# Kernel tuning notes

Hardware: AMD Instinct MI355X
Metric: run time of the kernel (lower is better)

Reference implementation:

```python
import jax, jax.numpy as jnp
import numpy as np

B, S, H, D = 2, 2048, 16, 128  # batch, seq, n_head, head_dim; n_embd = H*D
N_EMBD = H * D

def setup_inputs() -> dict:
    key = jax.random.key(0)
    kq, kk, kv = jax.random.split(key, 3)
    q = jax.random.normal(kq, (B, S, H, D), dtype=jnp.float32)
    k = jax.random.normal(kk, (B, S, H, D), dtype=jnp.float32)
    v = jax.random.normal(kv, (B, S, H, D), dtype=jnp.float32)
    return {"q": q, "k": k, "v": v}

def reference(q, k, v):
    # [B,S,H,D] -> [B,H,S,D]
    qh = jnp.transpose(q, (0, 2, 1, 3))
    kh = jnp.transpose(k, (0, 2, 1, 3))
    vh = jnp.transpose(v, (0, 2, 1, 3))
    # scores scaled by head_dim (NOT sqrt), matching the original module
    att = jnp.einsum('bhqd,bhkd->bhqk', qh, kh) / D
    att = jax.nn.softmax(att, axis=-1)
    y = jnp.einsum('bhqk,bhkd->bhqd', att, vh)
    # [B,H,S,D] -> [B,S,H,D] -> [B*S, n_embd]
    y = jnp.transpose(y, (0, 2, 1, 3)).reshape(B * S, N_EMBD)
    return y
```

## Files before the change

kernel.cpp:

```cpp
#include <hip/hip_runtime.h>


#define SEQ   2048
#define NHEAD 16
#define DH    128
#define NB    2
#define BQ    64
#define BK    64
#define NWAVE 4
#define NTHR  256
#define VSTR  72
#define PSTR  40
#define NKV   (SEQ / BK)
#define NELEM (NB * SEQ * NHEAD * DH)

typedef __attribute__((ext_vector_type(8))) short bf16x8;
typedef __attribute__((ext_vector_type(4))) float f32x4;

__device__ __forceinline__ unsigned short f2bf(float x) {
    unsigned int u = __builtin_bit_cast(unsigned int, x);
    u += 0x7fffu + ((u >> 16) & 1u);
    return (unsigned short)(u >> 16);
}

__global__ __launch_bounds__(256) void cvt_bf16(
    const float* __restrict__ q, const float* __restrict__ k,
    const float* __restrict__ v, unsigned short* __restrict__ dst)
{
    const int y = blockIdx.y;
    const float* s = (y == 0) ? q : (y == 1) ? k : v;
    unsigned short* d = dst + (size_t)y * NELEM;
    const int i = blockIdx.x * 256 + threadIdx.x;
    const float4 x = ((const float4*)s)[i];
    ushort4 o;
    o.x = f2bf(x.x); o.y = f2bf(x.y); o.z = f2bf(x.z); o.w = f2bf(x.w);
    ((ushort4*)d)[i] = o;
}

__global__ __launch_bounds__(NTHR, 4) void attn_fwd(
    const unsigned short* __restrict__ Qb,
    const unsigned short* __restrict__ Kb,
    const unsigned short* __restrict__ Vb,
    float* __restrict__ O)
{
    __shared__ unsigned short Kl[BK * DH];
    __shared__ unsigned short Vt[DH * VSTR];
    __shared__ unsigned short Pl[NWAVE * 16 * PSTR];

    const int tid  = threadIdx.x;
    const int wave = tid >> 6;
    const int lane = tid & 63;
    const int quad = lane >> 4;
    const int l16  = lane & 15;

    const int b  = blockIdx.y >> 4;
    const int h  = blockIdx.y & 15;
    const int q0 = blockIdx.x * BQ;

    const size_t rs = (size_t)NHEAD * DH;
    const unsigned short* qb = Qb + (size_t)b * SEQ * rs + (size_t)h * DH;
    const unsigned short* kb = Kb + (size_t)b * SEQ * rs + (size_t)h * DH;
    const unsigned short* vb = Vb + (size_t)b * SEQ * rs + (size_t)h * DH;

    bf16x8 qf[4];
    {
        const unsigned short* qp = qb + (size_t)(q0 + wave * 16 + l16) * rs + quad * 8;
        #pragma unroll
        for (int c = 0; c < 4; ++c)
            qf[c] = *(const bf16x8*)(qp + c * 32);
    }

    int koff[4];
    #pragma unroll
    for (int p = 0; p < 4; ++p) {
        const int cidx = (wave * 4 + p) * 64 + lane;
        const int r    = cidx >> 4;
        const int cc   = cidx & 15;
        const int gc   = cc ^ (r & 15);
        koff[p] = r * (int)rs + gc * 8;
    }

    const int kp = tid & 31;
    const int dc = tid >> 5;

    const f32x4 fzero = {0.f, 0.f, 0.f, 0.f};
    f32x4 o[8];
    #pragma unroll
    for (int t = 0; t < 8; ++t) o[t] = fzero;
    float lsum[4] = {0.f, 0.f, 0.f, 0.f};

    const float c1 = 1.44269504088896340736f / 128.0f;

    for (int kv = 0; kv < NKV; ++kv) {
        const int k0 = kv * BK;

        #pragma unroll
        for (int p = 0; p < 4; ++p) {
            const unsigned short* gp = kb + (size_t)k0 * rs + koff[p];
            __builtin_amdgcn_global_load_lds(
                (const __attribute__((address_space(1))) unsigned int*)gp,
                (__attribute__((address_space(3))) unsigned int*)&Kl[(wave * 4 + p) * 512],
                16, 0, 0);
        }
        {
            unsigned int* vw = (unsigned int*)Vt;
            #pragma unroll
            for (int p = 0; p < 2; ++p) {
                const int dcp = dc + p * 8;
                const unsigned short* src = vb + (size_t)(k0 + 2 * kp) * rs + dcp * 8;
                bf16x8 r0 = *(const bf16x8*)src;
                bf16x8 r1 = *(const bf16x8*)(src + rs);
                #pragma unroll
                for (int j = 0; j < 8; ++j) {
                    const unsigned int pr = ((unsigned int)(unsigned short)r0[j])
                                          | (((unsigned int)(unsigned short)r1[j]) << 16);
                    vw[(dcp * 8 + j) * (VSTR / 2) + kp] = pr;
                }
            }
        }
        __syncthreads();

        f32x4 s[4];
        #pragma unroll
        for (int t = 0; t < 4; ++t) s[t] = fzero;
        #pragma unroll
        for (int c = 0; c < 4; ++c) {
            #pragma unroll
            for (int t = 0; t < 4; ++t) {
                const int key = t * 16 + l16;
                bf16x8 kf = *(const bf16x8*)&Kl[key * DH + (((c * 4 + quad) ^ l16) << 3)];
                s[t] = __builtin_amdgcn_mfma_f32_16x16x32_bf16(qf[c], kf, s[t], 0, 0, 0);
            }
        }

        #pragma unroll
        for (int kc = 0; kc < 2; ++kc) {
            #pragma unroll
            for (int r = 0; r < 4; ++r) {
                const float e0 = __builtin_amdgcn_exp2f(s[kc * 2][r] * c1);
                const float e1 = __builtin_amdgcn_exp2f(s[kc * 2 + 1][r] * c1);
                lsum[r] += e0 + e1;
                const int prow = wave * 16 + quad * 4 + r;
                Pl[prow * PSTR + l16]      = (unsigned short)(__builtin_bit_cast(unsigned int, e0) >> 16);
                Pl[prow * PSTR + 16 + l16] = (unsigned short)(__builtin_bit_cast(unsigned int, e1) >> 16);
            }
            bf16x8 pf = *(const bf16x8*)&Pl[(wave * 16 + l16) * PSTR + quad * 8];
            #pragma unroll
            for (int t = 0; t < 8; ++t) {
                bf16x8 vf = *(const bf16x8*)&Vt[(t * 16 + l16) * VSTR + kc * 32 + quad * 8];
                o[t] = __builtin_amdgcn_mfma_f32_16x16x32_bf16(pf, vf, o[t], 0, 0, 0);
            }
        }
        __syncthreads();
    }

    #pragma unroll
    for (int r = 0; r < 4; ++r) {
        float l = lsum[r];
        l += __shfl_xor(l, 1, 64);
        l += __shfl_xor(l, 2, 64);
        l += __shfl_xor(l, 4, 64);
        l += __shfl_xor(l, 8, 64);
        const float inv = 1.0f / l;
        const int row = q0 + wave * 16 + quad * 4 + r;
        float* dst = O + (size_t)(b * SEQ + row) * rs + (size_t)h * DH;
        #pragma unroll
        for (int t = 0; t < 8; ++t)
            dst[t * 16 + l16] = o[t][r] * inv;
    }
}

extern "C" void kernel_launch(void* const* d_in, const int* in_sizes, int n_in,
                              void* d_out, int out_size, void* d_ws, size_t ws_size,
                              hipStream_t stream) {
    const float* q = (const float*)d_in[0];
    const float* k = (const float*)d_in[1];
    const float* v = (const float*)d_in[2];
    float* o = (float*)d_out;
    unsigned short* wsb = (unsigned short*)d_ws;

    cvt_bf16<<<dim3(NELEM / 1024, 3), 256, 0, stream>>>(q, k, v, wsb);
    attn_fwd<<<dim3(SEQ / BQ, NB * NHEAD), dim3(NTHR), 0, stream>>>(
        wsb, wsb + NELEM, wsb + 2 * (size_t)NELEM, o);
}
```

Before: 241.3 us.

## Switch attention to 32x32 MFMA with 128-row Q tiles and double-buffered K/V

Each workgroup now covers 128 query rows, with each wave owning 32 rows. QK^T and PV use 32x32x16 bf16 MFMA, computing S transposed so P is written per query row. K/V tiles are double-buffered in LDS, with next-tile global loads issued into registers before the current tile's compute, and only one barrier per iteration. This hides global load latency and improves MFMA efficiency. The cost is more registers and lower occupancy (launch bounds 2), a padded K layout in place of the XOR swizzle, and a wasted wraparound prefetch on the last iteration.

```diff
diff --git a/kernel.cpp b/kernel.cpp
--- a/kernel.cpp
+++ b/kernel.cpp
@@ -5,17 +5,17 @@
 #define NHEAD 16
 #define DH    128
 #define NB    2
-#define BQ    64
+#define BQ    128
 #define BK    64
-#define NWAVE 4
 #define NTHR  256
+#define KSTR  136
 #define VSTR  72
 #define PSTR  40
 #define NKV   (SEQ / BK)
 #define NELEM (NB * SEQ * NHEAD * DH)
 
-typedef __attribute__((ext_vector_type(8))) short bf16x8;
-typedef __attribute__((ext_vector_type(4))) float f32x4;
+typedef __attribute__((ext_vector_type(8)))  short bf16x8;
+typedef __attribute__((ext_vector_type(16))) float f32x16;
 
 __device__ __forceinline__ unsigned short f2bf(float x) {
     unsigned int u = __builtin_bit_cast(unsigned int, x);
@@ -37,21 +37,21 @@
     ((ushort4*)d)[i] = o;
 }
 
-__global__ __launch_bounds__(NTHR, 4) void attn_fwd(
+__global__ __launch_bounds__(NTHR, 2) void attn_fwd(
     const unsigned short* __restrict__ Qb,
     const unsigned short* __restrict__ Kb,
     const unsigned short* __restrict__ Vb,
     float* __restrict__ O)
 {
-    __shared__ unsigned short Kl[BK * DH];
-    __shared__ unsigned short Vt[DH * VSTR];
-    __shared__ unsigned short Pl[NWAVE * 16 * PSTR];
+    __shared__ unsigned short Kl[2][BK * KSTR];
+    __shared__ unsigned short Vl[2][DH * VSTR];
+    __shared__ unsigned short Pt[BQ * PSTR];
 
     const int tid  = threadIdx.x;
     const int wave = tid >> 6;
     const int lane = tid & 63;
-    const int quad = lane >> 4;
-    const int l16  = lane & 15;
+    const int hx   = lane >> 5;
+    const int l32  = lane & 31;
 
     const int b  = blockIdx.y >> 4;
     const int h  = blockIdx.y & 15;
@@ -62,111 +62,145 @@
     const unsigned short* kb = Kb + (size_t)b * SEQ * rs + (size_t)h * DH;
     const unsigned short* vb = Vb + (size_t)b * SEQ * rs + (size_t)h * DH;
 
-    bf16x8 qf[4];
+    bf16x8 qf[8];
     {
-        const unsigned short* qp = qb + (size_t)(q0 + wave * 16 + l16) * rs + quad * 8;
-        #pragma unroll
-        for (int c = 0; c < 4; ++c)
-            qf[c] = *(const bf16x8*)(qp + c * 32);
-    }
-
-    int koff[4];
+        const unsigned short* qp = qb + (size_t)(q0 + wave * 32 + l32) * rs + hx * 8;
+        #pragma unroll
+        for (int c = 0; c < 8; ++c)
+            qf[c] = *(const bf16x8*)(qp + c * 16);
+    }
+
+    int kgo[4], kls[4];
     #pragma unroll
     for (int p = 0; p < 4; ++p) {
         const int cidx = (wave * 4 + p) * 64 + lane;
-        const int r    = cidx >> 4;
+        const int key  = cidx >> 4;
         const int cc   = cidx & 15;
-        const int gc   = cc ^ (r & 15);
-        koff[p] = r * (int)rs + gc * 8;
-    }
-
-    const int kp = tid & 31;
-    const int dc = tid >> 5;
-
-    const f32x4 fzero = {0.f, 0.f, 0.f, 0.f};
-    f32x4 o[8];
-    #pragma unroll
-    for (int t = 0; t < 8; ++t) o[t] = fzero;
-    float lsum[4] = {0.f, 0.f, 0.f, 0.f};
-
+        kgo[p] = key * (int)rs + cc * 8;
+        kls[p] = key * KSTR + cc * 8;
+    }
+    const int kp  = tid & 31;
+    const int dcv = tid >> 5;
+
+    f32x16 o4[4];
+    #pragma unroll
+    for (int t = 0; t < 4; ++t)
+        #pragma unroll
+        for (int r = 0; r < 16; ++r) o4[t][r] = 0.f;
+    float lsum = 0.f;
     const float c1 = 1.44269504088896340736f / 128.0f;
 
+    bf16x8 kr[4], vr[4];
+
+    {
+        #pragma unroll
+        for (int p = 0; p < 4; ++p) kr[p] = *(const bf16x8*)(kb + kgo[p]);
+        #pragma unroll
+        for (int p = 0; p < 2; ++p) {
+            const unsigned short* src = vb + (size_t)(2 * kp) * rs + (dcv + p * 8) * 8;
+            vr[p * 2]     = *(const bf16x8*)src;
+            vr[p * 2 + 1] = *(const bf16x8*)(src + rs);
+        }
+        #pragma unroll
+        for (int p = 0; p < 4; ++p) *(bf16x8*)&Kl[0][kls[p]] = kr[p];
+        unsigned int* vw = (unsigned int*)&Vl[0][0];
+        #pragma unroll
+        for (int p = 0; p < 2; ++p)
+            #pragma unroll
+            for (int j = 0; j < 8; ++j) {
+                const unsigned int pr = ((unsigned int)(unsigned short)vr[p * 2][j])
+                                      | (((unsigned int)(unsigned short)vr[p * 2 + 1][j]) << 16);
+                vw[((dcv + p * 8) * 8 + j) * (VSTR / 2) + kp] = pr;
+            }
+    }
+    __syncthreads();
+
+    const int prow = (wave * 32 + l32) * PSTR;
+
     for (int kv = 0; kv < NKV; ++kv) {
-        const int k0 = kv * BK;
-
-        #pragma unroll
-        for (int p = 0; p < 4; ++p) {
-            const unsigned short* gp = kb + (size_t)k0 * rs + koff[p];
-            __builtin_amdgcn_global_load_lds(
-                (const __attribute__((address_space(1))) unsigned int*)gp,
-                (__attribute__((address_space(3))) unsigned int*)&Kl[(wave * 4 + p) * 512],
-                16, 0, 0);
-        }
+        const int cur = kv & 1;
+        const int k0n = ((kv + 1) & (NKV - 1)) * BK;
+
+        #pragma unroll
+        for (int p = 0; p < 4; ++p) kr[p] = *(const bf16x8*)(kb + (size_t)k0n * rs + kgo[p]);
+        #pragma unroll
+        for (int p = 0; p < 2; ++p) {
+            const unsigned short* src = vb + (size_t)(k0n + 2 * kp) * rs + (dcv + p * 8) * 8;
+            vr[p * 2]     = *(const bf16x8*)src;
+            vr[p * 2 + 1] = *(const bf16x8*)(src + rs);
+        }
+
+        const unsigned short* Kc = &Kl[cur][0];
+        const unsigned short* Vc = &Vl[cur][0];
+
+        #pragma unroll
+        for (int kt = 0; kt < 2; ++kt) {
+            f32x16 s;
+            #pragma unroll
+            for (int r = 0; r < 16; ++r) s[r] = 0.f;
+            #pragma unroll
+            for (int c = 0; c < 8; ++c) {
+                bf16x8 kf = *(const bf16x8*)&Kc[(kt * 32 + l32) * KSTR + c * 16 + hx * 8];
+                s = __builtin_amdgcn_mfma_f32_32x32x16_bf16(kf, qf[c], s, 0, 0, 0);
+            }
+            #pragma unroll
+            for (int g = 0; g < 4; ++g) {
+                const float e0 = __builtin_amdgcn_exp2f(s[g * 4 + 0] * c1);
+                const float e1 = __builtin_amdgcn_exp2f(s[g * 4 + 1] * c1);
+                const float e2 = __builtin_amdgcn_exp2f(s[g * 4 + 2] * c1);
+                const float e3 = __builtin_amdgcn_exp2f(s[g * 4 + 3] * c1);
+                lsum += (e0 + e1) + (e2 + e3);
+                ushort4 pk;
+                pk.x = (unsigned short)(__builtin_bit_cast(unsigned int, e0) >> 16);
+                pk.y = (unsigned short)(__builtin_bit_cast(unsigned int, e1) >> 16);
+                pk.z = (unsigned short)(__builtin_bit_cast(unsigned int, e2) >> 16);
+                pk.w = (unsigned short)(__builtin_bit_cast(unsigned int, e3) >> 16);
+                *(ushort4*)&Pt[prow + g * 8 + hx * 4] = pk;
+            }
+            #pragma unroll
+            for (int ks = 0; ks < 2; ++ks) {
+                bf16x8 pf = *(const bf16x8*)&Pt[prow + ks * 16 + hx * 8];
+                #pragma unroll
+                for (int dt = 0; dt < 4; ++dt) {
+                    bf16x8 vf = *(const bf16x8*)&Vc[(dt * 32 + l32) * VSTR
+                                                    + kt * 32 + ks * 16 + hx * 8];
+                    o4[dt] = __builtin_amdgcn_mfma_f32_32x32x16_bf16(pf, vf, o4[dt], 0, 0, 0);
+                }
+            }
+        }
+
+        const int nxt = cur ^ 1;
+        #pragma unroll
+        for (int p = 0; p < 4; ++p) *(bf16x8*)&Kl[nxt][kls[p]] = kr[p];
         {
-            unsigned int* vw = (unsigned int*)Vt;
-            #pragma unroll
-            for (int p = 0; p < 2; ++p) {
-                const int dcp = dc + p * 8;
-                const unsigned short* src = vb + (size_t)(k0 + 2 * kp) * rs + dcp * 8;
-                bf16x8 r0 = *(const bf16x8*)src;
-                bf16x8 r1 = *(const bf16x8*)(src + rs);
+            unsigned int* vw = (unsigned int*)&Vl[nxt][0];
+            #pragma unroll
+            for (int p = 0; p < 2; ++p)
                 #pragma unroll
                 for (int j = 0; j < 8; ++j) {
-                    const unsigned int pr = ((unsigned int)(unsigned short)r0[j])
-                                          | (((unsigned int)(unsigned short)r1[j]) << 16);
-                    vw[(dcp * 8 + j) * (VSTR / 2) + kp] = pr;
+                    const unsigned int pr = ((unsigned int)(unsigned short)vr[p * 2][j])
+                                          | (((unsigned int)(unsigned short)vr[p * 2 + 1][j]) << 16);
+                    vw[((dcv + p * 8) * 8 + j) * (VSTR / 2) + kp] = pr;
                 }
-            }
         }
         __syncthreads();
-
-        f32x4 s[4];
-        #pragma unroll
-        for (int t = 0; t < 4; ++t) s[t] = fzero;
-        #pragma unroll
-        for (int c = 0; c < 4; ++c) {
-            #pragma unroll
-            for (int t = 0; t < 4; ++t) {
-                const int key = t * 16 + l16;
-                bf16x8 kf = *(const bf16x8*)&Kl[key * DH + (((c * 4 + quad) ^ l16) << 3)];
-                s[t] = __builtin_amdgcn_mfma_f32_16x16x32_bf16(qf[c], kf, s[t], 0, 0, 0);
-            }
-        }
-
-        #pragma unroll
-        for (int kc = 0; kc < 2; ++kc) {
-            #pragma unroll
-            for (int r = 0; r < 4; ++r) {
-                const float e0 = __builtin_amdgcn_exp2f(s[kc * 2][r] * c1);
-                const float e1 = __builtin_amdgcn_exp2f(s[kc * 2 + 1][r] * c1);
-                lsum[r] += e0 + e1;
-                const int prow = wave * 16 + quad * 4 + r;
-                Pl[prow * PSTR + l16]      = (unsigned short)(__builtin_bit_cast(unsigned int, e0) >> 16);
-                Pl[prow * PSTR + 16 + l16] = (unsigned short)(__builtin_bit_cast(unsigned int, e1) >> 16);
-            }
-            bf16x8 pf = *(const bf16x8*)&Pl[(wave * 16 + l16) * PSTR + quad * 8];
-            #pragma unroll
-            for (int t = 0; t < 8; ++t) {
-                bf16x8 vf = *(const bf16x8*)&Vt[(t * 16 + l16) * VSTR + kc * 32 + quad * 8];
-                o[t] = __builtin_amdgcn_mfma_f32_16x16x32_bf16(pf, vf, o[t], 0, 0, 0);
-            }
-        }
-        __syncthreads();
-    }
-
-    #pragma unroll
-    for (int r = 0; r < 4; ++r) {
-        float l = lsum[r];
-        l += __shfl_xor(l, 1, 64);
-        l += __shfl_xor(l, 2, 64);
-        l += __shfl_xor(l, 4, 64);
-        l += __shfl_xor(l, 8, 64);
-        const float inv = 1.0f / l;
-        const int row = q0 + wave * 16 + quad * 4 + r;
-        float* dst = O + (size_t)(b * SEQ + row) * rs + (size_t)h * DH;
-        #pragma unroll
-        for (int t = 0; t < 8; ++t)
-            dst[t * 16 + l16] = o[t][r] * inv;
+    }
+
+    lsum += __shfl_xor(lsum, 32, 64);
+    const float inv = 1.0f / lsum;
+    float iv[16];
+    #pragma unroll
+    for (int r = 0; r < 16; ++r)
+        iv[r] = __shfl(inv, (r & 3) + 8 * (r >> 2) + 4 * hx, 64);
+
+    #pragma unroll
+    for (int dt = 0; dt < 4; ++dt) {
+        #pragma unroll
+        for (int r = 0; r < 16; ++r) {
+            const int ql = (r & 3) + 8 * (r >> 2) + 4 * hx;
+            const int qg = q0 + wave * 32 + ql;
+            O[(size_t)(b * SEQ + qg) * rs + (size_t)h * DH + dt * 32 + l32] = o4[dt][r] * iv[r];
+        }
     }
 }
 
```

Measured after the change: 213.2 us. 11.7% less time.
